# Kernel optimization log

Measured on AMD Instinct MI355X. Metric: run time of the kernel, lower is better.

The kernel has to match this reference:

```python
import jax, jax.numpy as jnp
import numpy as np

D_MODEL, D_FFN, N_EXPERTS, TOP_K = 1024, 4096, 8, 2
BATCH, SEQ = 4, 1024


def setup_inputs() -> dict:
    key = jax.random.key(0)
    kx, kr, k1, k2, k3 = jax.random.split(key, 5)
    scale = 0.02
    return {
        "x": jax.random.normal(kx, (BATCH, SEQ, D_MODEL), dtype=jnp.float32),
        "w_router": jax.random.normal(kr, (D_MODEL, N_EXPERTS), dtype=jnp.float32) * scale,
        "w1": jax.random.normal(k1, (N_EXPERTS, D_MODEL, D_FFN), dtype=jnp.float32) * scale,
        "w2": jax.random.normal(k2, (N_EXPERTS, D_FFN, D_MODEL), dtype=jnp.float32) * scale,
        "w3": jax.random.normal(k3, (N_EXPERTS, D_MODEL, D_FFN), dtype=jnp.float32) * scale,
    }


def reference(x, w_router, w1, w2, w3):
    B, S, D = x.shape
    E = w_router.shape[1]
    T = B * S
    xf = x.reshape(T, D)

    # --- router: softmax over experts, top-k, renormalize ---
    router_probs = jax.nn.softmax(xf @ w_router, axis=-1)          # (T, E)
    topk_probs, topk_idx = jax.lax.top_k(router_probs, TOP_K)      # (T, K)
    topk_probs = topk_probs / topk_probs.sum(axis=-1, keepdims=True)

    # per-token combine weight for each expert (top_k indices are distinct,
    # matching the torch per-slot accumulation exactly)
    comb = jnp.zeros((T, E), dtype=xf.dtype)
    comb = comb.at[jnp.arange(T)[:, None], topk_idx].add(topk_probs)  # (T, E)

    # --- dense SwiGLU experts (same math as masked loop) ---
    h = jnp.einsum("td,edf->tef", xf, w1)                          # (T, E, F)
    g = jnp.einsum("td,edf->tef", xf, w3)                          # (T, E, F)
    y = jnp.einsum("tef,efd->ted", jax.nn.silu(h) * g, w2)         # (T, E, D)
    out = jnp.einsum("te,ted->td", comb, y).reshape(B, S, D)

    # --- load-balance aux loss ---
    expert_mask = jax.nn.one_hot(topk_idx, E, dtype=jnp.float32).sum(axis=1)  # (T, E)
    tokens_per_expert = expert_mask.sum(axis=0) / T
    mean_probs = router_probs.mean(axis=0)
    aux_loss = E * jnp.sum(tokens_per_expert * mean_probs)
    return out, aux_loss
```

## Files before the change

kernel.cpp:

```cpp
#include <hip/hip_runtime.h>
#include <hip/hip_bf16.h>
#include <cstdint>
#include <cstddef>

#define TT 4096
#define DM 1024
#define DF 4096
#define NE 8
#define BTAB 72

typedef __attribute__((ext_vector_type(8))) short bf16x8;
typedef __attribute__((ext_vector_type(8))) unsigned short ushort8;
typedef __attribute__((ext_vector_type(4))) float f32x4;

static __device__ __forceinline__ unsigned short f2bf(float f) {
    union { float f; unsigned int u; } v; v.f = f;
    unsigned int u = v.u;
    return (unsigned short)((u + 0x7FFFu + ((u >> 16) & 1u)) >> 16);
}
static __device__ __forceinline__ float bf2f(unsigned short h) {
    union { unsigned int u; float f; } v; v.u = ((unsigned int)h) << 16;
    return v.f;
}

#define GLOAD16(gsrc, ldst)                                                        \
    __builtin_amdgcn_global_load_lds(                                              \
        (const __attribute__((address_space(1))) void*)(gsrc),                     \
        (__attribute__((address_space(3))) void*)(ldst), 16, 0, 0)

__global__ void transpose_v2(const float* __restrict__ in,
                             unsigned short* __restrict__ out,
                             int R, int C) {
    __shared__ float tile[64][65];
    const int e = blockIdx.z;
    const float* src = in + (size_t)e * R * C;
    unsigned short* dst = out + (size_t)e * R * C;
    const int c0 = blockIdx.x * 64, r0 = blockIdx.y * 64;
    const int tid = threadIdx.x;
    #pragma unroll
    for (int i = 0; i < 4; ++i) {
        int idx = tid + i * 256;
        int rr = idx >> 4, cc = idx & 15;
        float4 v = *(const float4*)(src + (size_t)(r0 + rr) * C + c0 + cc * 4);
        tile[rr][cc * 4 + 0] = v.x;
        tile[rr][cc * 4 + 1] = v.y;
        tile[rr][cc * 4 + 2] = v.z;
        tile[rr][cc * 4 + 3] = v.w;
    }
    __syncthreads();
    #pragma unroll
    for (int i = 0; i < 2; ++i) {
        int idx = tid + i * 256;
        int c = idx >> 3, rc = idx & 7;
        ushort8 o;
        #pragma unroll
        for (int j = 0; j < 8; ++j) o[j] = f2bf(tile[rc * 8 + j][c]);
        *(ushort8*)(dst + (size_t)(c0 + c) * R + r0 + rc * 8) = o;
    }
}

__global__ void router_kernel(const float* __restrict__ x,
                              const float* __restrict__ wr,
                              unsigned short* __restrict__ xb,
                              int* __restrict__ topi, float* __restrict__ topw,
                              float* __restrict__ probsum) {
    __shared__ float s_ps[NE];
    const int tid = threadIdx.x;
    if (tid < NE) s_ps[tid] = 0.f;
    __syncthreads();
    const int wid = tid >> 6, lane = tid & 63;
    const int t = blockIdx.x * 4 + wid;
    float acc[NE] = {0.f, 0.f, 0.f, 0.f, 0.f, 0.f, 0.f, 0.f};
    const float* xr = x + (size_t)t * DM;
    unsigned short* xbr = xb + (size_t)t * DM;
    for (int it = 0; it < DM / 64; ++it) {
        int d = it * 64 + lane;
        float xv = xr[d];
        xbr[d] = f2bf(xv);
        const float* w = wr + d * NE;
        #pragma unroll
        for (int e = 0; e < NE; ++e) acc[e] = fmaf(xv, w[e], acc[e]);
    }
    #pragma unroll
    for (int e = 0; e < NE; ++e) {
        float v = acc[e];
        #pragma unroll
        for (int off = 32; off; off >>= 1) v += __shfl_xor(v, off);
        acc[e] = v;
    }
    if (lane == 0) {
        float m = acc[0];
        #pragma unroll
        for (int e = 1; e < NE; ++e) m = fmaxf(m, acc[e]);
        float p[NE], s = 0.f;
        #pragma unroll
        for (int e = 0; e < NE; ++e) { p[e] = expf(acc[e] - m); s += p[e]; }
        float inv = 1.f / s;
        #pragma unroll
        for (int e = 0; e < NE; ++e) { p[e] *= inv; atomicAdd(&s_ps[e], p[e]); }
        int i1 = 0; float p1 = p[0];
        #pragma unroll
        for (int e = 1; e < NE; ++e) if (p[e] > p1) { p1 = p[e]; i1 = e; }
        int i2 = -1; float p2 = -1.f;
        #pragma unroll
        for (int e = 0; e < NE; ++e) if (e != i1 && p[e] > p2) { p2 = p[e]; i2 = e; }
        float rs = 1.f / (p1 + p2);
        topi[t * 2] = i1; topi[t * 2 + 1] = i2;
        topw[t * 2] = p1 * rs; topw[t * 2 + 1] = p2 * rs;
    }
    __syncthreads();
    if (tid < NE) atomicAdd(&probsum[tid], s_ps[tid]);
}

__global__ void assign_kernel(const int* __restrict__ topi,
                              int* __restrict__ list, int* __restrict__ slotpos,
                              int* __restrict__ cnt) {
    const int e = blockIdx.x;
    __shared__ int s_wc[4];
    const int tid = threadIdx.x, wid = tid >> 6, lane = tid & 63;
    int running = 0;
    for (int base = 0; base < TT; base += 256) {
        int t = base + tid;
        int hit = 0, slot = 0;
        int a = topi[2 * t], b = topi[2 * t + 1];
        if (a == e) { hit = 1; slot = 0; }
        else if (b == e) { hit = 1; slot = 1; }
        unsigned long long m = __ballot(hit);
        if (lane == 0) s_wc[wid] = __popcll(m);
        __syncthreads();
        int pre = 0, tot = 0;
        #pragma unroll
        for (int q = 0; q < 4; ++q) { int c = s_wc[q]; tot += c; if (q < wid) pre += c; }
        if (hit) {
            int pos = running + pre + __popcll(m & ((1ull << lane) - 1ull));
            list[e * TT + pos] = t;
            slotpos[2 * t + slot] = pos;
        }
        running += tot;
        __syncthreads();
    }
    if (tid == 0) cnt[e] = running;
}

__global__ void finalize_kernel(const int* __restrict__ cnt,
                                const float* __restrict__ probsum,
                                int* __restrict__ offs,
                                unsigned int* __restrict__ blocktab,
                                float* __restrict__ out_aux) {
    int o = 0;
    float aux = 0.f;
    int nb = 0;
    for (int e = 0; e < NE; ++e) {
        offs[e] = o; o += cnt[e];
        aux += (float)cnt[e] * probsum[e];
        int nrb = (cnt[e] + 127) >> 7;
        for (int rb = 0; rb < nrb; ++rb) blocktab[nb++] = ((unsigned)e << 16) | rb;
    }
    while (nb < BTAB) blocktab[nb++] = 0xFFFFFFFFu;
    *out_aux = (float)NE * aux / ((float)TT * (float)TT);
}

static __device__ __forceinline__ const bf16x8* frag_ptr(
        const unsigned short* base, int row, int ph16) {
    return (const bf16x8*)((const char*)base + row * 64 + ph16);
}

#define WAITBAR(N)                                                \
    asm volatile("s_waitcnt vmcnt(" #N ")" ::: "memory");         \
    __builtin_amdgcn_s_barrier();
#define ENDBAR                                                    \
    asm volatile("" ::: "memory");                                \
    __builtin_amdgcn_s_barrier();

__global__ __launch_bounds__(256, 2) void gemm1_kernel(
    const unsigned short* __restrict__ xb,
    const unsigned short* __restrict__ w1T,
    const unsigned short* __restrict__ w3T,
    unsigned short* __restrict__ act,
    const int* __restrict__ list,
    const int* __restrict__ cnt,
    const int* __restrict__ offs,
    const unsigned int* __restrict__ blocktab) {
    const unsigned int tab = blocktab[blockIdx.y];
    if (tab == 0xFFFFFFFFu) return;
    const int e = tab >> 16;
    const int rowbase = (int)(tab & 0xFFFFu) << 7;
    const int ce = cnt[e];
    const int fbase = blockIdx.x * 128;

    __shared__ __align__(16) unsigned short As[3 * 128 * 32];
    __shared__ __align__(16) unsigned short B1s[3 * 128 * 32];
    __shared__ __align__(16) unsigned short B3s[3 * 128 * 32];

    const int tid = threadIdx.x;
    const int lrow = tid >> 2;
    const int q = (tid & 3) ^ ((tid >> 3) & 3);

    int sp0 = rowbase + lrow;       if (sp0 >= ce) sp0 = ce - 1;
    int sp1 = rowbase + 64 + lrow;  if (sp1 >= ce) sp1 = ce - 1;
    const size_t tok0 = (size_t)list[e * TT + sp0];
    const size_t tok1 = (size_t)list[e * TT + sp1];

    const unsigned short* a0 = xb + tok0 * DM + q * 8;
    const unsigned short* a1 = xb + tok1 * DM + q * 8;
    const unsigned short* b1a = w1T + ((size_t)e * DF + fbase + lrow) * DM + q * 8;
    const unsigned short* b1b = b1a + (size_t)64 * DM;
    const unsigned short* b3a = w3T + ((size_t)e * DF + fbase + lrow) * DM + q * 8;
    const unsigned short* b3b = b3a + (size_t)64 * DM;

    char* ldsA  = (char*)As  + tid * 16;
    char* ldsB1 = (char*)B1s + tid * 16;
    char* ldsB3 = (char*)B3s + tid * 16;

    const int wid = tid >> 6, lane = tid & 63;
    const int wm = wid >> 1, wn = wid & 1;
    const int g = lane >> 4, r = lane & 15;
    const int ph16 = (g ^ ((r >> 1) & 3)) << 4;

    f32x4 acch[4][4] = {};
    f32x4 accg[4][4] = {};

#define STAGE1(T, BUF)                                   \
    {   const int koff = (T) * 32;                       \
        const int bo = (BUF) * 8192;                     \
        GLOAD16(a0 + koff,  ldsA + bo);                  \
        GLOAD16(a1 + koff,  ldsA + bo + 4096);           \
        GLOAD16(b1a + koff, ldsB1 + bo);                 \
        GLOAD16(b1b + koff, ldsB1 + bo + 4096);          \
        GLOAD16(b3a + koff, ldsB3 + bo);                 \
        GLOAD16(b3b + koff, ldsB3 + bo + 4096); }

#define COMP1(BS)                                                           \
    {   const unsigned short* Ac  = As  + (BS) * 4096;                      \
        const unsigned short* B1c = B1s + (BS) * 4096;                      \
        const unsigned short* B3c = B3s + (BS) * 4096;                      \
        bf16x8 af[4];                                                       \
        _Pragma("unroll") for (int m = 0; m < 4; ++m)                       \
            af[m] = *frag_ptr(Ac, wm * 64 + m * 16 + r, ph16);              \
        _Pragma("unroll") for (int n = 0; n < 4; ++n) {                     \
            bf16x8 f1 = *frag_ptr(B1c, wn * 64 + n * 16 + r, ph16);         \
            bf16x8 f3 = *frag_ptr(B3c, wn * 64 + n * 16 + r, ph16);         \
            _Pragma("unroll") for (int m = 0; m < 4; ++m) {                 \
                acch[m][n] = __builtin_amdgcn_mfma_f32_16x16x32_bf16(af[m], f1, acch[m][n], 0, 0, 0); \
                accg[m][n] = __builtin_amdgcn_mfma_f32_16x16x32_bf16(af[m], f3, accg[m][n], 0, 0, 0); } } }

    const int NT = DM / 32;
    STAGE1(0, 0);
    STAGE1(1, 1);
    int bs = 0, sb = 2;
    for (int t = 0; t < NT - 2; ++t) {
        STAGE1(t + 2, sb);
        WAITBAR(12)
        COMP1(bs)
        ENDBAR
        bs = (bs + 1 == 3) ? 0 : bs + 1;
        sb = (sb + 1 == 3) ? 0 : sb + 1;
    }
    WAITBAR(6)
    COMP1(bs)
    ENDBAR
    bs = (bs + 1 == 3) ? 0 : bs + 1;
    WAITBAR(0)
    COMP1(bs)
#undef STAGE1
#undef COMP1

    const int ob = offs[e];
    #pragma unroll
    for (int m = 0; m < 4; ++m) {
        #pragma unroll
        for (int j = 0; j < 4; ++j) {
            const int pos = rowbase + wm * 64 + m * 16 + g * 4 + j;
            if (pos < ce) {
                unsigned short* arow = act + (size_t)(ob + pos) * DF + fbase + wn * 64;
                #pragma unroll
                for (int n = 0; n < 4; ++n) {
                    float h = acch[m][n][j];
                    float gv = accg[m][n][j];
                    float a = (h / (1.f + __expf(-h))) * gv;
                    arow[n * 16 + r] = f2bf(a);
                }
            }
        }
    }
}

__global__ __launch_bounds__(256, 3) void gemm2_kernel(
    const unsigned short* __restrict__ act,
    const unsigned short* __restrict__ w2T,
    unsigned short* __restrict__ ybuf,
    const int* __restrict__ cnt,
    const int* __restrict__ offs,
    const unsigned int* __restrict__ blocktab) {
    const unsigned int tab = blocktab[blockIdx.y];
    if (tab == 0xFFFFFFFFu) return;
    const int e = tab >> 16;
    const int rowbase = (int)(tab & 0xFFFFu) << 7;
    const int ce = cnt[e];
    const int dbase = blockIdx.x * 128;
    const int ob = offs[e];

    __shared__ __align__(16) unsigned short As[3 * 128 * 32];
    __shared__ __align__(16) unsigned short Bs[3 * 128 * 32];

    const int tid = threadIdx.x;
    const int lrow = tid >> 2;
    const int q = (tid & 3) ^ ((tid >> 3) & 3);

    int sp0 = rowbase + lrow;       if (sp0 >= ce) sp0 = ce - 1;
    int sp1 = rowbase + 64 + lrow;  if (sp1 >= ce) sp1 = ce - 1;

    const unsigned short* a0 = act + (size_t)(ob + sp0) * DF + q * 8;
    const unsigned short* a1 = act + (size_t)(ob + sp1) * DF + q * 8;
    const unsigned short* b0 = w2T + ((size_t)e * DM + dbase + lrow) * DF + q * 8;
    const unsigned short* b1 = b0 + (size_t)64 * DF;

    char* ldsA = (char*)As + tid * 16;
    char* ldsB = (char*)Bs + tid * 16;

    const int wid = tid >> 6, lane = tid & 63;
    const int wm = wid >> 1, wn = wid & 1;
    const int g = lane >> 4, r = lane & 15;
    const int ph16 = (g ^ ((r >> 1) & 3)) << 4;

    f32x4 acc[4][4] = {};

#define STAGE2(T, BUF)                                   \
    {   const int koff = (T) * 32;                       \
        const int bo = (BUF) * 8192;                     \
        GLOAD16(a0 + koff, ldsA + bo);                   \
        GLOAD16(a1 + koff, ldsA + bo + 4096);            \
        GLOAD16(b0 + koff, ldsB + bo);                   \
        GLOAD16(b1 + koff, ldsB + bo + 4096); }

#define COMP2(BS)                                                           \
    {   const unsigned short* Ac = As + (BS) * 4096;                        \
        const unsigned short* Bc = Bs + (BS) * 4096;                        \
        bf16x8 af[4];                                                       \
        _Pragma("unroll") for (int m = 0; m < 4; ++m)                       \
            af[m] = *frag_ptr(Ac, wm * 64 + m * 16 + r, ph16);              \
        _Pragma("unroll") for (int n = 0; n < 4; ++n) {                     \
            bf16x8 bfr = *frag_ptr(Bc, wn * 64 + n * 16 + r, ph16);         \
            _Pragma("unroll") for (int m = 0; m < 4; ++m)                   \
                acc[m][n] = __builtin_amdgcn_mfma_f32_16x16x32_bf16(af[m], bfr, acc[m][n], 0, 0, 0); } }

    const int NT = DF / 32;
    STAGE2(0, 0);
    STAGE2(1, 1);
    int bs = 0, sb = 2;
    for (int t = 0; t < NT - 2; ++t) {
        STAGE2(t + 2, sb);
        WAITBAR(8)
        COMP2(bs)
        ENDBAR
        bs = (bs + 1 == 3) ? 0 : bs + 1;
        sb = (sb + 1 == 3) ? 0 : sb + 1;
    }
    WAITBAR(4)
    COMP2(bs)
    ENDBAR
    bs = (bs + 1 == 3) ? 0 : bs + 1;
    WAITBAR(0)
    COMP2(bs)
#undef STAGE2
#undef COMP2

    #pragma unroll
    for (int m = 0; m < 4; ++m) {
        #pragma unroll
        for (int j = 0; j < 4; ++j) {
            const int pos = rowbase + wm * 64 + m * 16 + g * 4 + j;
            if (pos < ce) {
                unsigned short* yrow = ybuf + (size_t)(ob + pos) * DM + dbase + wn * 64;
                #pragma unroll
                for (int n = 0; n < 4; ++n)
                    yrow[n * 16 + r] = f2bf(acc[m][n][j]);
            }
        }
    }
}

__global__ void combine_kernel(const unsigned short* __restrict__ ybuf,
                               const int* __restrict__ topi,
                               const float* __restrict__ topw,
                               const int* __restrict__ slotpos,
                               const int* __restrict__ offs,
                               float* __restrict__ out) {
    const int t = blockIdx.x;
    const int tid = threadIdx.x;
    const int e0 = topi[2 * t], e1 = topi[2 * t + 1];
    const int r0 = offs[e0] + slotpos[2 * t];
    const int r1 = offs[e1] + slotpos[2 * t + 1];
    const float w0 = topw[2 * t], w1 = topw[2 * t + 1];
    ushort4 a = *(const ushort4*)(ybuf + (size_t)r0 * DM + tid * 4);
    ushort4 b = *(const ushort4*)(ybuf + (size_t)r1 * DM + tid * 4);
    float4 o;
    o.x = w0 * bf2f(a.x) + w1 * bf2f(b.x);
    o.y = w0 * bf2f(a.y) + w1 * bf2f(b.y);
    o.z = w0 * bf2f(a.z) + w1 * bf2f(b.z);
    o.w = w0 * bf2f(a.w) + w1 * bf2f(b.w);
    *(float4*)(out + (size_t)t * DM + tid * 4) = o;
}

extern "C" void kernel_launch(void* const* d_in, const int* in_sizes, int n_in,
                              void* d_out, int out_size, void* d_ws, size_t ws_size,
                              hipStream_t stream) {
    (void)in_sizes; (void)n_in; (void)ws_size;
    const float* x  = (const float*)d_in[0];
    const float* wr = (const float*)d_in[1];
    const float* w1 = (const float*)d_in[2];
    const float* w2 = (const float*)d_in[3];
    const float* w3 = (const float*)d_in[4];
    float* out = (float*)d_out;

    char* ws = (char*)d_ws;
    size_t off = 0;
    auto alloc = [&](size_t bytes) -> void* {
        void* p = ws + off;
        off = (off + bytes + 255) & ~(size_t)255;
        return p;
    };
    unsigned short* w1T = (unsigned short*)alloc((size_t)NE * DF * DM * 2);
    unsigned short* w3T = (unsigned short*)alloc((size_t)NE * DF * DM * 2);
    unsigned short* w2T = (unsigned short*)alloc((size_t)NE * DM * DF * 2);
    unsigned short* act = (unsigned short*)alloc((size_t)2 * TT * DF * 2);
    unsigned short* xb  = (unsigned short*)alloc((size_t)TT * DM * 2);
    int*   topi    = (int*)alloc(TT * 2 * sizeof(int));
    float* topw    = (float*)alloc(TT * 2 * sizeof(float));
    int*   list    = (int*)alloc((size_t)NE * TT * sizeof(int));
    int*   slotpos = (int*)alloc(TT * 2 * sizeof(int));
    int*   cnt     = (int*)alloc(NE * sizeof(int));
    int*   offs    = (int*)alloc(NE * sizeof(int));
    float* probsum = (float*)alloc(NE * sizeof(float));
    unsigned int* blocktab = (unsigned int*)alloc(BTAB * sizeof(unsigned int));
    unsigned short* ybuf = w1T;

    hipMemsetAsync(probsum, 0, NE * sizeof(float), stream);

    dim3 tb(256);
    transpose_v2<<<dim3(DF / 64, DM / 64, NE), tb, 0, stream>>>(w1, w1T, DM, DF);
    transpose_v2<<<dim3(DF / 64, DM / 64, NE), tb, 0, stream>>>(w3, w3T, DM, DF);
    transpose_v2<<<dim3(DM / 64, DF / 64, NE), tb, 0, stream>>>(w2, w2T, DF, DM);

    router_kernel<<<TT / 4, 256, 0, stream>>>(x, wr, xb, topi, topw, probsum);
    assign_kernel<<<NE, 256, 0, stream>>>(topi, list, slotpos, cnt);
    finalize_kernel<<<1, 1, 0, stream>>>(cnt, probsum, offs, blocktab, out + (out_size - 1));

    gemm1_kernel<<<dim3(DF / 128, BTAB), 256, 0, stream>>>(xb, w1T, w3T, act, list, cnt, offs, blocktab);
    gemm2_kernel<<<dim3(DM / 128, BTAB), 256, 0, stream>>>(act, w2T, ybuf, cnt, offs, blocktab);
    combine_kernel<<<TT, 256, 0, stream>>>(ybuf, topi, topw, slotpos, offs, out);
}
```

Measured before the change: 465.7 us.

## Rewrite gemm1 with 256x256 tiles, 512 threads, interleaved w1/w3 and ping-pong schedule

gemm1 now processes 256 token rows per block with 512 threads, and its B tile interleaves w1 and w3 columns so one accumulator array holds both h and g. It uses a double-buffered 128KB LDS stage with K-steps of 64 and a phased schedule that alternates barriers, MFMA bursts under raised priority, and async global-to-LDS loads. A second block table with 256-row granularity is built in finalize_kernel to drive the new grid. The aim is higher arithmetic intensity per LDS byte and better overlap of loads with MFMA. The cost is lower occupancy and more wasted rows on partially filled expert tiles.

```diff
diff --git a/kernel.cpp b/kernel.cpp
--- a/kernel.cpp
+++ b/kernel.cpp
@@ -8,6 +8,7 @@
 #define DF 4096
 #define NE 8
 #define BTAB 72
+#define BTAB2 40
 
 typedef __attribute__((ext_vector_type(8))) short bf16x8;
 typedef __attribute__((ext_vector_type(8))) unsigned short ushort8;
@@ -146,33 +147,25 @@
                                 const float* __restrict__ probsum,
                                 int* __restrict__ offs,
                                 unsigned int* __restrict__ blocktab,
+                                unsigned int* __restrict__ blocktab2,
                                 float* __restrict__ out_aux) {
     int o = 0;
     float aux = 0.f;
-    int nb = 0;
+    int nb = 0, nb2 = 0;
     for (int e = 0; e < NE; ++e) {
         offs[e] = o; o += cnt[e];
         aux += (float)cnt[e] * probsum[e];
         int nrb = (cnt[e] + 127) >> 7;
         for (int rb = 0; rb < nrb; ++rb) blocktab[nb++] = ((unsigned)e << 16) | rb;
+        int nrb2 = (cnt[e] + 255) >> 8;
+        for (int rb = 0; rb < nrb2; ++rb) blocktab2[nb2++] = ((unsigned)e << 16) | rb;
     }
     while (nb < BTAB) blocktab[nb++] = 0xFFFFFFFFu;
+    while (nb2 < BTAB2) blocktab2[nb2++] = 0xFFFFFFFFu;
     *out_aux = (float)NE * aux / ((float)TT * (float)TT);
 }
 
-static __device__ __forceinline__ const bf16x8* frag_ptr(
-        const unsigned short* base, int row, int ph16) {
-    return (const bf16x8*)((const char*)base + row * 64 + ph16);
-}
-
-#define WAITBAR(N)                                                \
-    asm volatile("s_waitcnt vmcnt(" #N ")" ::: "memory");         \
-    __builtin_amdgcn_s_barrier();
-#define ENDBAR                                                    \
-    asm volatile("" ::: "memory");                                \
-    __builtin_amdgcn_s_barrier();
-
-__global__ __launch_bounds__(256, 2) void gemm1_kernel(
+__global__ __launch_bounds__(512, 2) void gemm1_kernel(
     const unsigned short* __restrict__ xb,
     const unsigned short* __restrict__ w1T,
     const unsigned short* __restrict__ w3T,
@@ -180,109 +173,135 @@
     const int* __restrict__ list,
     const int* __restrict__ cnt,
     const int* __restrict__ offs,
-    const unsigned int* __restrict__ blocktab) {
-    const unsigned int tab = blocktab[blockIdx.y];
+    const unsigned int* __restrict__ blocktab2) {
+    const unsigned int tab = blocktab2[blockIdx.y];
     if (tab == 0xFFFFFFFFu) return;
     const int e = tab >> 16;
-    const int rowbase = (int)(tab & 0xFFFFu) << 7;
+    const int rowbase = (int)(tab & 0xFFFFu) << 8;
     const int ce = cnt[e];
     const int fbase = blockIdx.x * 128;
 
-    __shared__ __align__(16) unsigned short As[3 * 128 * 32];
-    __shared__ __align__(16) unsigned short B1s[3 * 128 * 32];
-    __shared__ __align__(16) unsigned short B3s[3 * 128 * 32];
+    __shared__ __align__(16) unsigned short lds[65536];
+    char* ldsC = (char*)lds;
 
     const int tid = threadIdx.x;
-    const int lrow = tid >> 2;
-    const int q = (tid & 3) ^ ((tid >> 3) & 3);
-
-    int sp0 = rowbase + lrow;       if (sp0 >= ce) sp0 = ce - 1;
-    int sp1 = rowbase + 64 + lrow;  if (sp1 >= ce) sp1 = ce - 1;
-    const size_t tok0 = (size_t)list[e * TT + sp0];
-    const size_t tok1 = (size_t)list[e * TT + sp1];
-
-    const unsigned short* a0 = xb + tok0 * DM + q * 8;
-    const unsigned short* a1 = xb + tok1 * DM + q * 8;
-    const unsigned short* b1a = w1T + ((size_t)e * DF + fbase + lrow) * DM + q * 8;
-    const unsigned short* b1b = b1a + (size_t)64 * DM;
-    const unsigned short* b3a = w3T + ((size_t)e * DF + fbase + lrow) * DM + q * 8;
-    const unsigned short* b3b = b3a + (size_t)64 * DM;
-
-    char* ldsA  = (char*)As  + tid * 16;
-    char* ldsB1 = (char*)B1s + tid * 16;
-    char* ldsB3 = (char*)B3s + tid * 16;
-
-    const int wid = tid >> 6, lane = tid & 63;
-    const int wm = wid >> 1, wn = wid & 1;
-    const int g = lane >> 4, r = lane & 15;
-    const int ph16 = (g ^ ((r >> 1) & 3)) << 4;
-
-    f32x4 acch[4][4] = {};
-    f32x4 accg[4][4] = {};
-
-#define STAGE1(T, BUF)                                   \
-    {   const int koff = (T) * 32;                       \
-        const int bo = (BUF) * 8192;                     \
-        GLOAD16(a0 + koff,  ldsA + bo);                  \
-        GLOAD16(a1 + koff,  ldsA + bo + 4096);           \
-        GLOAD16(b1a + koff, ldsB1 + bo);                 \
-        GLOAD16(b1b + koff, ldsB1 + bo + 4096);          \
-        GLOAD16(b3a + koff, ldsB3 + bo);                 \
-        GLOAD16(b3b + koff, ldsB3 + bo + 4096); }
-
-#define COMP1(BS)                                                           \
-    {   const unsigned short* Ac  = As  + (BS) * 4096;                      \
-        const unsigned short* B1c = B1s + (BS) * 4096;                      \
-        const unsigned short* B3c = B3s + (BS) * 4096;                      \
-        bf16x8 af[4];                                                       \
-        _Pragma("unroll") for (int m = 0; m < 4; ++m)                       \
-            af[m] = *frag_ptr(Ac, wm * 64 + m * 16 + r, ph16);              \
-        _Pragma("unroll") for (int n = 0; n < 4; ++n) {                     \
-            bf16x8 f1 = *frag_ptr(B1c, wn * 64 + n * 16 + r, ph16);         \
-            bf16x8 f3 = *frag_ptr(B3c, wn * 64 + n * 16 + r, ph16);         \
-            _Pragma("unroll") for (int m = 0; m < 4; ++m) {                 \
-                acch[m][n] = __builtin_amdgcn_mfma_f32_16x16x32_bf16(af[m], f1, acch[m][n], 0, 0, 0); \
-                accg[m][n] = __builtin_amdgcn_mfma_f32_16x16x32_bf16(af[m], f3, accg[m][n], 0, 0, 0); } } }
-
-    const int NT = DM / 32;
-    STAGE1(0, 0);
-    STAGE1(1, 1);
-    int bs = 0, sb = 2;
-    for (int t = 0; t < NT - 2; ++t) {
-        STAGE1(t + 2, sb);
-        WAITBAR(12)
-        COMP1(bs)
-        ENDBAR
-        bs = (bs + 1 == 3) ? 0 : bs + 1;
-        sb = (sb + 1 == 3) ? 0 : sb + 1;
-    }
-    WAITBAR(6)
-    COMP1(bs)
-    ENDBAR
-    bs = (bs + 1 == 3) ? 0 : bs + 1;
-    WAITBAR(0)
-    COMP1(bs)
-#undef STAGE1
-#undef COMP1
+    const int lane = tid & 63, wid = tid >> 6;
+    const int wm = wid >> 2, wn = wid & 3;
+
+    const unsigned short* aP[2][2];
+    const unsigned short* bP[2][2];
+    #pragma unroll
+    for (int ci = 0; ci < 2; ++ci) {
+        const int c = tid + ci * 512;
+        const int r = (c >> 2) & 15, rg = c >> 7, cc = c & 3, ks = (c >> 6) & 1;
+        const int row = rg * 16 + r;
+        const int kb = ks * 64 + ((cc * 16) ^ ((r & 8) << 2));
+        #pragma unroll
+        for (int h = 0; h < 2; ++h) {
+            int sp = rowbase + h * 128 + row; if (sp >= ce) sp = ce - 1;
+            aP[h][ci] = xb + (size_t)list[e * TT + sp] * DM + (kb >> 1);
+            const int n = h * 128 + row;
+            const int col = fbase + (n >> 5) * 16 + (n & 15);
+            const unsigned short* wsrc = ((n >> 4) & 1) ? w3T : w1T;
+            bP[h][ci] = wsrc + ((size_t)e * DF + col) * DM + (kb >> 1);
+        }
+    }
+
+#define STG_A(H, T, B) {                                                          \
+    GLOAD16(aP[H][0] + (size_t)(T) * 64, ldsC + (B) * 65536 + (H) * 16384 + tid * 16);        \
+    GLOAD16(aP[H][1] + (size_t)(T) * 64, ldsC + (B) * 65536 + (H) * 16384 + 8192 + tid * 16); }
+#define STG_B(H, T, B) {                                                          \
+    GLOAD16(bP[H][0] + (size_t)(T) * 64, ldsC + (B) * 65536 + 32768 + (H) * 16384 + tid * 16);        \
+    GLOAD16(bP[H][1] + (size_t)(T) * 64, ldsC + (B) * 65536 + 32768 + (H) * 16384 + 8192 + tid * 16); }
+
+    const int lofs = ((lane & 15) << 6) + ((((lane >> 4) << 4) ^ ((lane & 8) << 2)));
+
+#define RDA(BB, MQ) { _Pragma("unroll") for (int i = 0; i < 4; ++i) {             \
+    _Pragma("unroll") for (int k2 = 0; k2 < 2; ++k2)                              \
+        aq[i][k2] = *(const bf16x8*)(ldsC + (BB) + wm * 16384 +                   \
+                     (((MQ) * 4 + i) * 2 + k2) * 1024 + lofs); } }
+#define RDB(DST, BB, NQ) { _Pragma("unroll") for (int u = 0; u < 2; ++u) {        \
+    _Pragma("unroll") for (int k2 = 0; k2 < 2; ++k2)                              \
+        DST[u][k2] = *(const bf16x8*)(ldsC + (BB) + 32768 + (wn >> 1) * 16384 +   \
+                     (wn & 1) * 8192 + ((NQ) * 2 + u) * 2048 + k2 * 1024 + lofs); } }
+#define MMQ(MQ, NQ, BQ) { __builtin_amdgcn_s_setprio(1);                          \
+    _Pragma("unroll") for (int i = 0; i < 4; ++i)                                 \
+    _Pragma("unroll") for (int u = 0; u < 2; ++u)                                 \
+    _Pragma("unroll") for (int k2 = 0; k2 < 2; ++k2)                              \
+        acc[(MQ) * 4 + i][(NQ) * 2 + u] = __builtin_amdgcn_mfma_f32_16x16x32_bf16(\
+            aq[i][k2], BQ[u][k2], acc[(MQ) * 4 + i][(NQ) * 2 + u], 0, 0, 0);      \
+    __builtin_amdgcn_s_setprio(0); }
+
+    f32x4 acc[8][4] = {};
+    bf16x8 aq[4][2], b0[2][2], b1[2][2];
+
+    STG_A(0, 0, 0); STG_A(1, 0, 0); STG_B(0, 0, 0); STG_B(1, 0, 0);
+    STG_B(0, 1, 1); STG_B(1, 1, 1); STG_A(0, 1, 1);
+    asm volatile("s_waitcnt vmcnt(6)" ::: "memory");
+    __builtin_amdgcn_s_barrier();
+
+    #pragma unroll 1
+    for (int h = 0; h < 16; ++h) {
+        const int bb = (h & 1) * 65536;
+        RDA(bb, 0) RDB(b0, bb, 0)
+        if (h < 15) STG_A(1, h + 1, (h & 1) ^ 1);
+        __builtin_amdgcn_s_barrier();
+        __builtin_amdgcn_sched_barrier(0);
+        MMQ(0, 0, b0)
+        __builtin_amdgcn_sched_barrier(0);
+        __builtin_amdgcn_s_barrier();
+        RDB(b1, bb, 1)
+        __builtin_amdgcn_s_barrier();
+        __builtin_amdgcn_sched_barrier(0);
+        MMQ(0, 1, b1)
+        __builtin_amdgcn_sched_barrier(0);
+        __builtin_amdgcn_s_barrier();
+        RDA(bb, 1)
+        if (h < 14) STG_B(0, h + 2, h & 1);
+        __builtin_amdgcn_s_barrier();
+        __builtin_amdgcn_sched_barrier(0);
+        MMQ(1, 0, b0)
+        __builtin_amdgcn_sched_barrier(0);
+        __builtin_amdgcn_s_barrier();
+        if (h < 14) { STG_B(1, h + 2, h & 1); STG_A(0, h + 2, h & 1); }
+        __builtin_amdgcn_s_barrier();
+        __builtin_amdgcn_sched_barrier(0);
+        MMQ(1, 1, b1)
+        __builtin_amdgcn_sched_barrier(0);
+        if (h < 14)       { asm volatile("s_waitcnt vmcnt(6)" ::: "memory"); }
+        else if (h == 14) { asm volatile("s_waitcnt vmcnt(0)" ::: "memory"); }
+        __builtin_amdgcn_s_barrier();
+    }
+#undef STG_A
+#undef STG_B
+#undef RDA
+#undef RDB
+#undef MMQ
 
     const int ob = offs[e];
-    #pragma unroll
-    for (int m = 0; m < 4; ++m) {
+    const int g = lane >> 4, rr = lane & 15;
+    #pragma unroll
+    for (int m = 0; m < 8; ++m) {
         #pragma unroll
         for (int j = 0; j < 4; ++j) {
-            const int pos = rowbase + wm * 64 + m * 16 + g * 4 + j;
+            const int pos = rowbase + wm * 128 + m * 16 + g * 4 + j;
             if (pos < ce) {
-                unsigned short* arow = act + (size_t)(ob + pos) * DF + fbase + wn * 64;
+                unsigned short* arow = act + (size_t)(ob + pos) * DF + fbase + wn * 32;
                 #pragma unroll
-                for (int n = 0; n < 4; ++n) {
-                    float h = acch[m][n][j];
-                    float gv = accg[m][n][j];
-                    float a = (h / (1.f + __expf(-h))) * gv;
-                    arow[n * 16 + r] = f2bf(a);
+                for (int p = 0; p < 2; ++p) {
+                    float hv = acc[m][2 * p][j];
+                    float gv = acc[m][2 * p + 1][j];
+                    float a = (hv / (1.f + __expf(-hv))) * gv;
+                    arow[p * 16 + rr] = f2bf(a);
                 }
             }
         }
     }
+}
+
+static __device__ __forceinline__ const bf16x8* frag_ptr(
+        const unsigned short* base, int row, int ph16) {
+    return (const bf16x8*)((const char*)base + row * 64 + ph16);
 }
 
 __global__ __launch_bounds__(256, 3) void gemm2_kernel(
@@ -350,17 +369,22 @@
     int bs = 0, sb = 2;
     for (int t = 0; t < NT - 2; ++t) {
         STAGE2(t + 2, sb);
-        WAITBAR(8)
+        asm volatile("s_waitcnt vmcnt(8)" ::: "memory");
+        __builtin_amdgcn_s_barrier();
         COMP2(bs)
-        ENDBAR
+        asm volatile("" ::: "memory");
+        __builtin_amdgcn_s_barrier();
         bs = (bs + 1 == 3) ? 0 : bs + 1;
         sb = (sb + 1 == 3) ? 0 : sb + 1;
     }
-    WAITBAR(4)
+    asm volatile("s_waitcnt vmcnt(4)" ::: "memory");
+    __builtin_amdgcn_s_barrier();
     COMP2(bs)
-    ENDBAR
+    asm volatile("" ::: "memory");
+    __builtin_amdgcn_s_barrier();
     bs = (bs + 1 == 3) ? 0 : bs + 1;
-    WAITBAR(0)
+    asm volatile("s_waitcnt vmcnt(0)" ::: "memory");
+    __builtin_amdgcn_s_barrier();
     COMP2(bs)
 #undef STAGE2
 #undef COMP2
@@ -432,7 +456,8 @@
     int*   cnt     = (int*)alloc(NE * sizeof(int));
     int*   offs    = (int*)alloc(NE * sizeof(int));
     float* probsum = (float*)alloc(NE * sizeof(float));
-    unsigned int* blocktab = (unsigned int*)alloc(BTAB * sizeof(unsigned int));
+    unsigned int* blocktab  = (unsigned int*)alloc(BTAB * sizeof(unsigned int));
+    unsigned int* blocktab2 = (unsigned int*)alloc(BTAB2 * sizeof(unsigned int));
     unsigned short* ybuf = w1T;
 
     hipMemsetAsync(probsum, 0, NE * sizeof(float), stream);
@@ -444,9 +469,9 @@
 
     router_kernel<<<TT / 4, 256, 0, stream>>>(x, wr, xb, topi, topw, probsum);
     assign_kernel<<<NE, 256, 0, stream>>>(topi, list, slotpos, cnt);
-    finalize_kernel<<<1, 1, 0, stream>>>(cnt, probsum, offs, blocktab, out + (out_size - 1));
-
-    gemm1_kernel<<<dim3(DF / 128, BTAB), 256, 0, stream>>>(xb, w1T, w3T, act, list, cnt, offs, blocktab);
+    finalize_kernel<<<1, 1, 0, stream>>>(cnt, probsum, offs, blocktab, blocktab2, out + (out_size - 1));
+
+    gemm1_kernel<<<dim3(DF / 128, BTAB2), 512, 0, stream>>>(xb, w1T, w3T, act, list, cnt, offs, blocktab2);
     gemm2_kernel<<<dim3(DM / 128, BTAB), 256, 0, stream>>>(act, w2T, ybuf, cnt, offs, blocktab);
     combine_kernel<<<TT, 256, 0, stream>>>(ybuf, topi, topw, slotpos, offs, out);
 }
```

New measurement: 443.1 us. 1.05x faster.
